# Performance work log

Measured on AMD Instinct MI355X. Metric: run time of the kernel, lower is better.

Reference implementation:

```python
import jax, jax.numpy as jnp
import numpy as np

N_PIX = 65536   # 256x256 render
N_GAUSS = 2048
N_COL = 3


def setup_inputs() -> dict:
    key = jax.random.key(0)
    k1, k2, k3, k4 = jax.random.split(key, 4)
    x = jax.random.uniform(k1, (N_PIX, 2), dtype=jnp.float32)           # pixel coords
    mus = jax.random.uniform(k2, (N_GAUSS, 2), dtype=jnp.float32)       # Gaussian means
    # SPD covariances: A A^T + sigma*I  (small spatial extent ~0.05)
    A = jax.random.normal(k3, (N_GAUSS, 2, 2), dtype=jnp.float32) * 0.05
    covs = jnp.einsum('mij,mkj->mik', A, A) + 0.01 * jnp.eye(2, dtype=jnp.float32)
    cols = jax.random.uniform(k4, (N_GAUSS, N_COL), dtype=jnp.float32)  # RGB per Gaussian
    return {"x": x, "mus": mus, "covs": covs, "cols": cols}


def reference(x, mus, covs, cols):
    # d: [N, M, 2] pixel-to-mean offsets
    d = x[:, None, :] - mus[None, :, :]
    # solve(covs, d) per (pixel, Gaussian) == cov_inv @ d; covs depend only on Gaussian,
    # so invert once per Gaussian (same math as torch.linalg.solve per pair).
    cov_inv = jnp.linalg.inv(covs)                      # [M, 2, 2]
    maha = jnp.einsum('nmi,mij,nmj->nm', d, cov_inv, d)  # [N, M] Mahalanobis distances
    w = jnp.exp(-0.5 * maha)                             # [N, M] Gaussian weights
    # weighted sum of colors over Gaussians: [N, M] @ [M, 3] -> [N, 3]
    return jnp.einsum('nm,mc->nc', w, cols)
```

## Files before the change

### kernel.cpp

```cpp
#include <hip/hip_runtime.h>

#define N_PIX   65536
#define N_GAUSS 2048

typedef __bf16 bf16x8 __attribute__((ext_vector_type(8)));
typedef float  f32x4  __attribute__((ext_vector_type(4)));

union BF8U { uint4 u; bf16x8 h; };
__device__ inline bf16x8 as_bf(uint4 u) { BF8U x; x.u = u; return x.h; }

__device__ inline unsigned short bfbits(float f) {
  __bf16 h = (__bf16)f;
  return __builtin_bit_cast(unsigned short, h);
}
__device__ inline float bf2f(unsigned short b) {
  return (float)__builtin_bit_cast(__bf16, b);
}
__device__ inline unsigned pkb(unsigned short a, unsigned short b) {
  return (unsigned)a | ((unsigned)b << 16);
}
__device__ inline unsigned pk2f(float a, float b) {
  return pkb(bfbits(a), bfbits(b));
}


__global__ __launch_bounds__(256) void prep_kernel(
    const float* __restrict__ mus, const float* __restrict__ covs,
    const float* __restrict__ cols, uint4* __restrict__ ws) {
  int tid = blockIdx.x * 256 + threadIdx.x;
  if (tid < 8192) {
    int lane = tid & 63;
    int tile = tid >> 6;
    int grp  = lane >> 4;
    int g    = tile * 16 + (lane & 15);
    float c00 = covs[4*g+0], c01 = covs[4*g+1];
    float c10 = covs[4*g+2], c11 = covs[4*g+3];
    float inv_det = 1.0f / (c00*c11 - c01*c10);
    float ia =  c11 * inv_det;
    float ib = -c01 * inv_det;
    float ic =  c00 * inv_det;
    float mx = mus[2*g+0], my = mus[2*g+1];
    const float kk = -0.7213475204444817f;
    float coef[6];
    coef[0] = kk * ia;
    coef[1] = kk * 2.0f * ib;
    coef[2] = kk * ic;
    coef[3] = -2.0f * kk * (ia*mx + ib*my);
    coef[4] = -2.0f * kk * (ib*mx + ic*my);
    coef[5] = kk * (ia*mx*mx + 2.0f*ib*mx*my + ic*my*my);
    unsigned short ch[6], cl[6];
    #pragma unroll
    for (int i = 0; i < 6; ++i) {
      ch[i] = bfbits(coef[i]);
      cl[i] = bfbits(coef[i] - bf2f(ch[i]));
    }
    uint4 v = make_uint4(0,0,0,0);
    if (grp == 0)      v = make_uint4(pkb(ch[0],ch[1]), pkb(ch[2],ch[3]), pkb(ch[4],ch[5]), pkb(cl[0],cl[1]));
    else if (grp == 1) v = make_uint4(pkb(cl[2],cl[3]), pkb(cl[4],cl[5]), pkb(ch[0],ch[1]), pkb(ch[2],ch[3]));
    else if (grp == 2) v = make_uint4(pkb(ch[4],ch[5]), pkb(cl[0],cl[1]), pkb(cl[2],cl[3]), pkb(cl[4],cl[5]));
    ws[tid] = v;
  } else if (tid < 12288) {
    int t2   = tid - 8192;
    int lane = t2 & 63;
    int tile = t2 >> 6;
    int rgb  = lane & 15;
    int grp  = lane >> 4;
    uint4 v = make_uint4(0,0,0,0);
    if (rgb < 3) {
      unsigned short b[8];
      #pragma unroll
      for (int j = 0; j < 8; ++j) {
        int sig = 4*grp + (j & 3) + ((j >> 2) ? 16 : 0);
        b[j] = bfbits(cols[(tile*32 + sig)*3 + rgb]);
      }
      v = make_uint4(pkb(b[0],b[1]), pkb(b[2],b[3]), pkb(b[4],b[5]), pkb(b[6],b[7]));
    }
    ws[8192 + t2] = v;
  }
}

__global__ __launch_bounds__(512, 4) void render_kernel(
    const float2* __restrict__ x, const uint4* __restrict__ ws,
    float* __restrict__ out) {
  const uint4* gq  = ws;
  const uint4* pvc = ws + 8192;

  int tid  = threadIdx.x;
  int lane = tid & 63;
  int c    = lane & 15, grp = lane >> 4;
  int wave = tid >> 6;
  int wpix = blockIdx.x * 128 + wave * 16;

  float2 p = x[wpix + c];
  float mono[6] = {p.x*p.x, p.x*p.y, p.y*p.y, p.x, p.y, 1.0f};
  unsigned short ph[6], pl[6];
  #pragma unroll
  for (int i = 0; i < 6; ++i) {
    ph[i] = bfbits(mono[i]);
    pl[i] = bfbits(mono[i] - bf2f(ph[i]));
  }
  uint4 pv4 = make_uint4(0,0,0,0);
  if (grp == 0)      pv4 = make_uint4(pkb(ph[0],ph[1]), pkb(ph[2],ph[3]), pkb(ph[4],ph[5]), pkb(ph[0],ph[1]));
  else if (grp == 1) pv4 = make_uint4(pkb(ph[2],ph[3]), pkb(ph[4],ph[5]), pkb(pl[0],pl[1]), pkb(pl[2],pl[3]));
  else if (grp == 2) pv4 = make_uint4(pkb(pl[4],pl[5]), pkb(pl[0],pl[1]), pkb(pl[2],pl[3]), pkb(pl[4],pl[5]));
  bf16x8 pf = as_bf(pv4);

  f32x4 acc  = {0.f, 0.f, 0.f, 0.f};
  const f32x4 zero = {0.f, 0.f, 0.f, 0.f};

  for (int chk = 0; chk < 8; ++chk) {
    uint4 cf[8];
    #pragma unroll
    for (int t = 0; t < 8; ++t)
      cf[t] = pvc[chk*512 + t*64 + lane];
    #pragma unroll
    for (int pr = 0; pr < 8; ++pr) {
      uint4 ga = gq[chk*1024 + pr*128 + lane];
      uint4 gb = gq[chk*1024 + pr*128 + 64 + lane];
      f32x4 q0 = __builtin_amdgcn_mfma_f32_16x16x32_bf16(as_bf(ga), pf, zero, 0, 0, 0);
      f32x4 q1 = __builtin_amdgcn_mfma_f32_16x16x32_bf16(as_bf(gb), pf, zero, 0, 0, 0);
      unsigned w0 = pk2f(__builtin_amdgcn_exp2f(q0[0]), __builtin_amdgcn_exp2f(q0[1]));
      unsigned w1 = pk2f(__builtin_amdgcn_exp2f(q0[2]), __builtin_amdgcn_exp2f(q0[3]));
      unsigned w2 = pk2f(__builtin_amdgcn_exp2f(q1[0]), __builtin_amdgcn_exp2f(q1[1]));
      unsigned w3 = pk2f(__builtin_amdgcn_exp2f(q1[2]), __builtin_amdgcn_exp2f(q1[3]));
      uint4 wf = make_uint4(w0, w1, w2, w3);
      acc = __builtin_amdgcn_mfma_f32_16x16x32_bf16(as_bf(cf[pr]), as_bf(wf), acc, 0, 0, 0);
    }
  }
  if (grp == 0) {
    int pix = wpix + c;
    out[pix*3 + 0] = acc[0];
    out[pix*3 + 1] = acc[1];
    out[pix*3 + 2] = acc[2];
  }
}

extern "C" void kernel_launch(void* const* d_in, const int* in_sizes, int n_in,
                              void* d_out, int out_size, void* d_ws, size_t ws_size,
                              hipStream_t stream) {
  const float* x    = (const float*)d_in[0];
  const float* mus  = (const float*)d_in[1];
  const float* covs = (const float*)d_in[2];
  const float* cols = (const float*)d_in[3];
  float* out = (float*)d_out;
  uint4* ws  = (uint4*)d_ws;

  prep_kernel<<<48, 256, 0, stream>>>(mus, covs, cols, ws);
  render_kernel<<<512, 512, 0, stream>>>((const float2*)x, ws, out);
}
```

Baseline: 84.81 us.

## Split Gaussian range across two blocks and stage coefficients in LDS via global_load_lds

Doubles the grid so each block handles half of the Gaussian chunks for its 128 pixels, and combines the partial results with atomic adds into an output zeroed by a memset. Gaussian coefficient tiles are double-buffered into shared memory with direct global-to-LDS loads, and the launch bound asks for higher occupancy. The goal is more parallelism and latency hiding on a grid of only 512 blocks. The cost is an extra memset, atomics on the output, block-level syncs per chunk, and float summation order that is no longer deterministic.

```diff
diff --git a/kernel.cpp b/kernel.cpp
--- a/kernel.cpp
+++ b/kernel.cpp
@@ -79,9 +79,25 @@
   }
 }
 
-__global__ __launch_bounds__(512, 4) void render_kernel(
+__device__ inline bf16x8 make_pf(float2 p, int grp) {
+  float mono[6] = {p.x*p.x, p.x*p.y, p.y*p.y, p.x, p.y, 1.0f};
+  unsigned short ph[6], pl[6];
+  #pragma unroll
+  for (int i = 0; i < 6; ++i) {
+    ph[i] = bfbits(mono[i]);
+    pl[i] = bfbits(mono[i] - bf2f(ph[i]));
+  }
+  uint4 v = make_uint4(0,0,0,0);
+  if (grp == 0)      v = make_uint4(pkb(ph[0],ph[1]), pkb(ph[2],ph[3]), pkb(ph[4],ph[5]), pkb(ph[0],ph[1]));
+  else if (grp == 1) v = make_uint4(pkb(ph[2],ph[3]), pkb(ph[4],ph[5]), pkb(pl[0],pl[1]), pkb(pl[2],pl[3]));
+  else if (grp == 2) v = make_uint4(pkb(pl[4],pl[5]), pkb(pl[0],pl[1]), pkb(pl[2],pl[3]), pkb(pl[4],pl[5]));
+  return as_bf(v);
+}
+
+__global__ __launch_bounds__(512, 8) void render_kernel(
     const float2* __restrict__ x, const uint4* __restrict__ ws,
     float* __restrict__ out) {
+  __shared__ uint4 smem[2048];
   const uint4* gq  = ws;
   const uint4* pvc = ws + 8192;
 
@@ -89,34 +105,38 @@
   int lane = tid & 63;
   int c    = lane & 15, grp = lane >> 4;
   int wave = tid >> 6;
-  int wpix = blockIdx.x * 128 + wave * 16;
+  int pixblk = blockIdx.x & 511;
+  int half   = blockIdx.x >> 9;
+  int cbase  = half * 4;
+  int wpix = pixblk * 128 + wave * 16;
 
-  float2 p = x[wpix + c];
-  float mono[6] = {p.x*p.x, p.x*p.y, p.y*p.y, p.x, p.y, 1.0f};
-  unsigned short ph[6], pl[6];
-  #pragma unroll
-  for (int i = 0; i < 6; ++i) {
-    ph[i] = bfbits(mono[i]);
-    pl[i] = bfbits(mono[i] - bf2f(ph[i]));
-  }
-  uint4 pv4 = make_uint4(0,0,0,0);
-  if (grp == 0)      pv4 = make_uint4(pkb(ph[0],ph[1]), pkb(ph[2],ph[3]), pkb(ph[4],ph[5]), pkb(ph[0],ph[1]));
-  else if (grp == 1) pv4 = make_uint4(pkb(ph[2],ph[3]), pkb(ph[4],ph[5]), pkb(pl[0],pl[1]), pkb(pl[2],pl[3]));
-  else if (grp == 2) pv4 = make_uint4(pkb(pl[4],pl[5]), pkb(pl[0],pl[1]), pkb(pl[2],pl[3]), pkb(pl[4],pl[5]));
-  bf16x8 pf = as_bf(pv4);
+  bf16x8 pf = make_pf(x[wpix + c], grp);
 
   f32x4 acc  = {0.f, 0.f, 0.f, 0.f};
   const f32x4 zero = {0.f, 0.f, 0.f, 0.f};
 
-  for (int chk = 0; chk < 8; ++chk) {
-    uint4 cf[8];
-    #pragma unroll
-    for (int t = 0; t < 8; ++t)
-      cf[t] = pvc[chk*512 + t*64 + lane];
+#define STAGE(DSTBUF, CHK) do {                                               \
+    __builtin_amdgcn_global_load_lds(                                         \
+      (const __attribute__((address_space(1))) void*)(gq + (CHK)*1024 + tid), \
+      (__attribute__((address_space(3))) void*)(&smem[(DSTBUF)*1024 + tid]),  \
+      16, 0, 0);                                                              \
+    __builtin_amdgcn_global_load_lds(                                         \
+      (const __attribute__((address_space(1))) void*)(gq + (CHK)*1024 + 512 + tid), \
+      (__attribute__((address_space(3))) void*)(&smem[(DSTBUF)*1024 + 512 + tid]),  \
+      16, 0, 0);                                                              \
+  } while (0)
+
+  STAGE(0, cbase);
+  __syncthreads();
+  #pragma unroll
+  for (int chk = 0; chk < 4; ++chk) {
+    int buf = chk & 1;
+    if (chk < 3) STAGE(buf ^ 1, cbase + chk + 1);
     #pragma unroll
     for (int pr = 0; pr < 8; ++pr) {
-      uint4 ga = gq[chk*1024 + pr*128 + lane];
-      uint4 gb = gq[chk*1024 + pr*128 + 64 + lane];
+      uint4 ga = smem[buf*1024 + (2*pr+0)*64 + lane];
+      uint4 gb = smem[buf*1024 + (2*pr+1)*64 + lane];
+      uint4 cf = pvc[(cbase+chk)*512 + pr*64 + lane];
       f32x4 q0 = __builtin_amdgcn_mfma_f32_16x16x32_bf16(as_bf(ga), pf, zero, 0, 0, 0);
       f32x4 q1 = __builtin_amdgcn_mfma_f32_16x16x32_bf16(as_bf(gb), pf, zero, 0, 0, 0);
       unsigned w0 = pk2f(__builtin_amdgcn_exp2f(q0[0]), __builtin_amdgcn_exp2f(q0[1]));
@@ -124,14 +144,17 @@
       unsigned w2 = pk2f(__builtin_amdgcn_exp2f(q1[0]), __builtin_amdgcn_exp2f(q1[1]));
       unsigned w3 = pk2f(__builtin_amdgcn_exp2f(q1[2]), __builtin_amdgcn_exp2f(q1[3]));
       uint4 wf = make_uint4(w0, w1, w2, w3);
-      acc = __builtin_amdgcn_mfma_f32_16x16x32_bf16(as_bf(cf[pr]), as_bf(wf), acc, 0, 0, 0);
+      acc = __builtin_amdgcn_mfma_f32_16x16x32_bf16(as_bf(cf), as_bf(wf), acc, 0, 0, 0);
     }
+    __syncthreads();
   }
+#undef STAGE
+
   if (grp == 0) {
     int pix = wpix + c;
-    out[pix*3 + 0] = acc[0];
-    out[pix*3 + 1] = acc[1];
-    out[pix*3 + 2] = acc[2];
+    unsafeAtomicAdd(&out[pix*3 + 0], acc[0]);
+    unsafeAtomicAdd(&out[pix*3 + 1], acc[1]);
+    unsafeAtomicAdd(&out[pix*3 + 2], acc[2]);
   }
 }
 
@@ -145,6 +168,8 @@
   float* out = (float*)d_out;
   uint4* ws  = (uint4*)d_ws;
 
+  hipMemsetAsync(out, 0, (size_t)out_size * sizeof(float), stream);
+
   prep_kernel<<<48, 256, 0, stream>>>(mus, covs, cols, ws);
-  render_kernel<<<512, 512, 0, stream>>>((const float2*)x, ws, out);
+  render_kernel<<<1024, 512, 0, stream>>>((const float2*)x, ws, out);
 }
```

After: 83.58 us. No clear change (-1.4%).
